# Kernel tuning notes

Measured on AMD Instinct MI355X. Metric: run time of the kernel, lower is better.

Reference implementation:

```python
import jax, jax.numpy as jnp
import numpy as np

D_MODEL = 2048
N_HEADS = 16
D_HEAD = D_MODEL // N_HEADS
BATCH = 4
SEQ = 2048


def setup_inputs() -> dict:
    key = jax.random.key(0)
    ks = jax.random.split(key, 10)
    s = 1.0 / np.sqrt(D_MODEL)
    inp = {
        "x": jax.random.normal(ks[0], (BATCH, SEQ, D_MODEL), dtype=jnp.float32),
        "attn_mask": jnp.ones((1, 1, SEQ, SEQ), dtype=jnp.int32),
        "Wq": jax.random.uniform(ks[1], (D_MODEL, D_MODEL), jnp.float32, -s, s),
        "bq": jax.random.uniform(ks[2], (D_MODEL,), jnp.float32, -s, s),
        "Wk": jax.random.uniform(ks[3], (D_MODEL, D_MODEL), jnp.float32, -s, s),
        "bk": jax.random.uniform(ks[4], (D_MODEL,), jnp.float32, -s, s),
        "Wv": jax.random.uniform(ks[5], (D_MODEL, D_MODEL), jnp.float32, -s, s),
        "bv": jax.random.uniform(ks[6], (D_MODEL,), jnp.float32, -s, s),
        "Wo": jax.random.uniform(ks[7], (D_MODEL, D_MODEL), jnp.float32, -s, s),
        "bo": jax.random.uniform(ks[8], (D_MODEL,), jnp.float32, -s, s),
    }
    return inp


def reference(x, attn_mask, Wq, bq, Wk, bk, Wv, bv, Wo, bo):
    B, S, D = x.shape
    # projections (torch Linear: x @ W.T + b); split heads -> (B, H, S, Dh)
    def split(t):
        return t.reshape(B, S, N_HEADS, D_HEAD).transpose(0, 2, 1, 3)
    q = split(x @ Wq.T + bq)
    k = split(x @ Wk.T + bk)
    v = split(x @ Wv.T + bv)
    scale = 1.0 / np.sqrt(D_HEAD).astype(np.float32)
    scores = jnp.einsum('bhqd,bhkd->bhqk', q, k) * scale  # (B,H,S,S)
    scores = jnp.where(attn_mask == 0, jnp.float32(-jnp.inf), scores)
    attn = jax.nn.softmax(scores, axis=-1)
    out = jnp.einsum('bhqk,bhkd->bhqd', attn, v)  # (B,H,S,Dh)
    out = out.transpose(0, 2, 1, 3).reshape(B, S, D)
    return out @ Wo.T + bo
```

## Files before the change

### kernel.cpp

```cpp
#include <hip/hip_runtime.h>
#include <stdint.h>
#include <stddef.h>

typedef __attribute__((ext_vector_type(8))) short short8;
typedef __attribute__((ext_vector_type(4))) float f32x4;

#define SEQ    2048
#define DMODEL 2048
#define NHEAD  16
#define DHEAD  128
#define BATCH  4
#define KVT    32
#define NKVT   (SEQ / KVT)

__device__ __forceinline__ unsigned short f2b(float f) {
  unsigned int u;
  __builtin_memcpy(&u, &f, sizeof(u));
  u = u + 0x7FFFu + ((u >> 16) & 1u);
  return (unsigned short)(u >> 16);
}

__device__ __forceinline__ void gload16(const void* g, void* l) {
  __builtin_amdgcn_global_load_lds(
      (const __attribute__((address_space(1))) unsigned int*)g,
      (__attribute__((address_space(3))) unsigned int*)l, 16, 0, 0);
}


__global__ __launch_bounds__(256) void cvt_x_kernel(
    const float* __restrict__ src, unsigned short* __restrict__ dst, int n8)
{
  const int idx = blockIdx.x * 256 + threadIdx.x;
  if (idx >= n8) return;
  const f32x4 a = *(const f32x4*)(src + (size_t)idx * 8);
  const f32x4 b = *(const f32x4*)(src + (size_t)idx * 8 + 4);
  short8 o;
  o[0] = (short)f2b(a[0]); o[1] = (short)f2b(a[1]);
  o[2] = (short)f2b(a[2]); o[3] = (short)f2b(a[3]);
  o[4] = (short)f2b(b[0]); o[5] = (short)f2b(b[1]);
  o[6] = (short)f2b(b[2]); o[7] = (short)f2b(b[3]);
  const int i = idx >> 8;
  const int k = (idx & 255) * 8;
  const size_t e = ((size_t)(i >> 4) * 64 + (k >> 5)) * 512
                 + (((k >> 3) & 3) * 16 + (i & 15)) * 8;
  *(short8*)(dst + e) = o;
}

__global__ __launch_bounds__(256) void cvt_w_kernel(
    const float* __restrict__ s0, const float* __restrict__ s1,
    const float* __restrict__ s2, const float* __restrict__ s3,
    unsigned short* __restrict__ dst, int n8)
{
  const int y = blockIdx.y;
  const float* src = (y == 0) ? s0 : (y == 1) ? s1 : (y == 2) ? s2 : s3;
  unsigned short* d = dst + (size_t)y * DMODEL * DMODEL;
  const int idx = blockIdx.x * 256 + threadIdx.x;
  if (idx >= n8) return;
  const f32x4 a = *(const f32x4*)(src + (size_t)idx * 8);
  const f32x4 b = *(const f32x4*)(src + (size_t)idx * 8 + 4);
  short8 o;
  o[0] = (short)f2b(a[0]); o[1] = (short)f2b(a[1]);
  o[2] = (short)f2b(a[2]); o[3] = (short)f2b(a[3]);
  o[4] = (short)f2b(b[0]); o[5] = (short)f2b(b[1]);
  o[6] = (short)f2b(b[2]); o[7] = (short)f2b(b[3]);
  const int i = idx >> 8;
  const int k = (idx & 255) * 8;
  const size_t e = ((size_t)(i >> 4) * 64 + (k >> 5)) * 512
                 + (((k >> 3) & 3) * 16 + (i & 15)) * 8;
  *(short8*)(d + e) = o;
}

__global__ __launch_bounds__(512, 2) void gemm_bt_kernel(
    const unsigned short* __restrict__ A,
    const unsigned short* __restrict__ W0, const unsigned short* __restrict__ W1,
    const unsigned short* __restrict__ W2,
    const float* __restrict__ b0, const float* __restrict__ b1,
    const float* __restrict__ b2,
    unsigned short* __restrict__ o0, unsigned short* __restrict__ o1,
    unsigned short* __restrict__ o2,
    float* __restrict__ of,
    int mode_base)
{
  const int z = blockIdx.z;
  const unsigned short* W    = (z == 0) ? W0 : (z == 1) ? W1 : W2;
  const float* bias          = (z == 0) ? b0 : (z == 1) ? b1 : b2;
  unsigned short* out        = (z == 0) ? o0 : (z == 1) ? o1 : o2;
  const int mode = mode_base + z;

  const int mt = blockIdx.x * 4 + (blockIdx.y & 3);
  const int nt = blockIdx.y >> 2;
  const int m0 = mt * 256;
  const int n0 = nt * 256;

  __shared__ __align__(16) unsigned short LA[4][8192];
  __shared__ __align__(16) unsigned short LB[4][8192];

  const int tid = threadIdx.x;
  const int wid = tid >> 6;
  const int ln  = tid & 63;
  const int l15 = ln & 15;
  const int lg  = ln >> 4;
  const int wr  = wid >> 2;
  const int wc  = wid & 3;

  const unsigned short* sA = A + ((size_t)((m0 >> 4) + wid) * 64) * 512 + ln * 8;
  const unsigned short* sB = W + ((size_t)((n0 >> 4) + wid) * 64) * 512 + ln * 8;
  const size_t FROW8 = (size_t)8 * 64 * 512;

  auto stage = [&](int kt) {
    unsigned short* dA = &LA[kt & 3][wid * 512 + ln * 8];
    unsigned short* dB = &LB[kt & 3][wid * 512 + ln * 8];
    gload16(sA + (size_t)kt * 512,         dA);
    gload16(sA + FROW8 + (size_t)kt * 512, dA + 8 * 512);
    gload16(sB + (size_t)kt * 512,         dB);
    gload16(sB + FROW8 + (size_t)kt * 512, dB + 8 * 512);
  };

  f32x4 acc[8][4];
#pragma unroll
  for (int m = 0; m < 8; ++m)
#pragma unroll
    for (int n = 0; n < 4; ++n) acc[m][n] = (f32x4){0.f, 0.f, 0.f, 0.f};

  stage(0); stage(1); stage(2);
  asm volatile("s_waitcnt vmcnt(8)" ::: "memory");
  __builtin_amdgcn_s_barrier();
  asm volatile("" ::: "memory");

  for (int j = 0; j < 64; ++j) {
    const int buf = j & 3;

    short8 bfr[4], a[8];
#pragma unroll
    for (int ni = 0; ni < 4; ++ni)
      bfr[ni] = *(const short8*)(&LB[buf][(wc * 4 + ni) * 512 + ln * 8]);
#pragma unroll
    for (int mi = 0; mi < 8; ++mi)
      a[mi] = *(const short8*)(&LA[buf][(wr * 8 + mi) * 512 + ln * 8]);

    if (j + 3 < 64) stage(j + 3);

    __builtin_amdgcn_s_setprio(1);
#pragma unroll
    for (int mi = 0; mi < 8; ++mi)
#pragma unroll
      for (int ni = 0; ni < 4; ++ni)
        acc[mi][ni] = __builtin_amdgcn_mfma_f32_16x16x32_bf16(a[mi], bfr[ni], acc[mi][ni], 0, 0, 0);
    __builtin_amdgcn_s_setprio(0);

    if (j <= 60)      asm volatile("s_waitcnt vmcnt(8)" ::: "memory");
    else if (j == 61) asm volatile("s_waitcnt vmcnt(4)" ::: "memory");
    else if (j == 62) asm volatile("s_waitcnt vmcnt(0)" ::: "memory");
    asm volatile("" ::: "memory");
    __builtin_amdgcn_s_barrier();
    asm volatile("" ::: "memory");
  }

#pragma unroll
  for (int n = 0; n < 4; ++n) {
    const int jj = n0 + wc * 64 + n * 16 + l15;
    const float bb = bias[jj];
#pragma unroll
    for (int m = 0; m < 8; ++m) {
#pragma unroll
      for (int r = 0; r < 4; ++r) {
        const int i = m0 + wr * 128 + m * 16 + lg * 4 + r;
        float v = acc[m][n][r] + bb;
        if (mode == 0) v *= 0.0883883476483184f;
        if (mode == 3) {
          of[(size_t)i * DMODEL + jj] = v;
        } else {
          const int b = i >> 11, s = i & 2047, hh = jj >> 7, dh = jj & 127;
          const size_t bhOff = (size_t)(b * 16 + hh) * (SEQ * DHEAD);
          size_t addr;
          if (mode == 0)
            addr = bhOff + (size_t)s * DHEAD + dh;
          else if (mode == 1)
            addr = bhOff + (size_t)(s >> 4) * 2048 + (dh >> 5) * 512
                 + ((dh >> 3) & 3) * 128 + (s & 15) * 8 + (dh & 7);
          else
            addr = bhOff + (size_t)(s >> 5) * 4096 + (dh >> 4) * 512
                 + ((s >> 3) & 3) * 128 + (dh & 15) * 8 + (s & 7);
          out[addr] = f2b(v);
        }
      }
    }
  }
}

__global__ __launch_bounds__(256, 4) void attn_kernel(
    const unsigned short* __restrict__ Q,
    const unsigned short* __restrict__ Kf,
    const unsigned short* __restrict__ Vf,
    unsigned short* __restrict__ AO)
{
  const int idx = blockIdx.x;
  const int xcd = idx & 7;
  const int sq  = idx >> 3;
  const int bh  = xcd * 8 + (sq >> 5);
  const int qt  = sq & 31;

  const int wave = threadIdx.x >> 6;
  const int lane = threadIdx.x & 63;
  const int l15  = lane & 15;
  const int lg   = lane >> 4;
  const int q0   = qt * 64 + wave * 16;

  const unsigned short* Qb = Q  + (size_t)bh * SEQ * DHEAD;
  const unsigned short* Kb = Kf + (size_t)bh * SEQ * DHEAD;
  const unsigned short* Vb = Vf + (size_t)bh * SEQ * DHEAD;

  __shared__ __align__(16) unsigned short Ks[2][4096];
  __shared__ __align__(16) unsigned short Vs[2][4096];
  __shared__ __align__(16) unsigned short P[4][16][40];

  short8 qf[4];
#pragma unroll
  for (int k = 0; k < 4; ++k)
    qf[k] = *(const short8*)(Qb + (size_t)(q0 + l15) * DHEAD + k * 32 + lg * 8);

  short8 onesf;
#pragma unroll
  for (int e = 0; e < 8; ++e) onesf[e] = (short)0x3F80;

  f32x4 oacc[9];
#pragma unroll
  for (int n = 0; n < 9; ++n) oacc[n] = (f32x4){0.f, 0.f, 0.f, 0.f};
  float mrun[4];
#pragma unroll
  for (int r = 0; r < 4; ++r) mrun[r] = -1e30f;

  const int t = threadIdx.x;
  auto STAGE = [&](int buf, int kvt) {
    const unsigned short* ksrc = Kb + (size_t)kvt * 4096;
    const unsigned short* vsrc = Vb + (size_t)kvt * 4096;
    gload16(ksrc + t * 8,        &Ks[buf][t * 8]);
    gload16(ksrc + 2048 + t * 8, &Ks[buf][2048 + t * 8]);
    gload16(vsrc + t * 8,        &Vs[buf][t * 8]);
    gload16(vsrc + 2048 + t * 8, &Vs[buf][2048 + t * 8]);
  };

  STAGE(0, 0);

  for (int kvt = 0; kvt < NKVT; ++kvt) {
    const int cur = kvt & 1;
    if (kvt + 1 < NKVT) {
      STAGE(cur ^ 1, kvt + 1);
      asm volatile("s_waitcnt vmcnt(4)" ::: "memory");
    } else {
      asm volatile("s_waitcnt vmcnt(0)" ::: "memory");
    }
    __builtin_amdgcn_s_barrier();
    __builtin_amdgcn_sched_barrier(0);

    f32x4 sacc[2];
#pragma unroll
    for (int n = 0; n < 2; ++n) sacc[n] = (f32x4){0.f, 0.f, 0.f, 0.f};
    __builtin_amdgcn_s_setprio(1);
#pragma unroll
    for (int n = 0; n < 2; ++n) {
#pragma unroll
      for (int k = 0; k < 4; ++k) {
        short8 kfr = *(const short8*)(&Ks[cur][n * 2048 + k * 512 + lane * 8]);
        sacc[n] = __builtin_amdgcn_mfma_f32_16x16x32_bf16(qf[k], kfr, sacc[n], 0, 0, 0);
      }
    }
    __builtin_amdgcn_s_setprio(0);

    float d = -1e30f;
#pragma unroll
    for (int r = 0; r < 4; ++r)
      d = fmaxf(d, fmaxf(sacc[0][r], sacc[1][r]) - mrun[r]);
    if (__any(d > 8.f)) {
#pragma unroll
      for (int r = 0; r < 4; ++r) {
        float m = fmaxf(sacc[0][r], sacc[1][r]);
        m = fmaxf(m, __shfl_xor(m, 1));
        m = fmaxf(m, __shfl_xor(m, 2));
        m = fmaxf(m, __shfl_xor(m, 4));
        m = fmaxf(m, __shfl_xor(m, 8));
        if (m > mrun[r]) {
          const float alpha = __expf(mrun[r] - m);
#pragma unroll
          for (int n = 0; n < 9; ++n) oacc[n][r] *= alpha;
          mrun[r] = m;
        }
      }
    }

#pragma unroll
    for (int n = 0; n < 2; ++n)
#pragma unroll
      for (int r = 0; r < 4; ++r)
        P[wave][lg * 4 + r][n * 16 + l15] =
            (unsigned short)f2b(__expf(sacc[n][r] - mrun[r]));
    asm volatile("s_waitcnt lgkmcnt(0)" ::: "memory");
    __builtin_amdgcn_sched_barrier(0);

    short8 pf = *(const short8*)(&P[wave][l15][lg * 8]);
    __builtin_amdgcn_s_setprio(1);
#pragma unroll
    for (int n = 0; n < 8; ++n) {
      short8 vfr = *(const short8*)(&Vs[cur][n * 512 + lane * 8]);
      oacc[n] = __builtin_amdgcn_mfma_f32_16x16x32_bf16(pf, vfr, oacc[n], 0, 0, 0);
    }
    oacc[8] = __builtin_amdgcn_mfma_f32_16x16x32_bf16(pf, onesf, oacc[8], 0, 0, 0);
    __builtin_amdgcn_s_setprio(0);

    asm volatile("s_waitcnt lgkmcnt(0)" ::: "memory");
    __builtin_amdgcn_s_barrier();
    __builtin_amdgcn_sched_barrier(0);
  }

  const int b = bh >> 4, h = bh & 15;
  float inv[4];
#pragma unroll
  for (int r = 0; r < 4; ++r) inv[r] = 1.f / oacc[8][r];
#pragma unroll
  for (int n = 0; n < 8; ++n) {
    const int kk  = h * 4 + (n >> 1);
    const int sub = (n * 2 + (l15 >> 3)) & 3;
#pragma unroll
    for (int r = 0; r < 4; ++r) {
      const int i = b * SEQ + q0 + lg * 4 + r;
      const size_t e = ((size_t)(i >> 4) * 64 + kk) * 512
                     + sub * 128 + (i & 15) * 8 + (l15 & 7);
      AO[e] = f2b(oacc[n][r] * inv[r]);
    }
  }
}

extern "C" void kernel_launch(void* const* d_in, const int* in_sizes, int n_in,
                              void* d_out, int out_size, void* d_ws, size_t ws_size,
                              hipStream_t stream)
{
  const float* xf  = (const float*)d_in[0];
  const float* Wqf = (const float*)d_in[2];
  const float* bq  = (const float*)d_in[3];
  const float* Wkf = (const float*)d_in[4];
  const float* bk  = (const float*)d_in[5];
  const float* Wvf = (const float*)d_in[6];
  const float* bv  = (const float*)d_in[7];
  const float* Wof = (const float*)d_in[8];
  const float* bo  = (const float*)d_in[9];
  float* out = (float*)d_out;

  const size_t QE = (size_t)64 * SEQ * DHEAD;
  const size_t WE = (size_t)DMODEL * DMODEL;

  unsigned short* Qw = (unsigned short*)d_out;
  unsigned short* Kw = Qw + QE;

  unsigned short* Vtw = (unsigned short*)d_ws;
  unsigned short* AOw = Vtw + QE;
  unsigned short* xb  = AOw + QE;
  unsigned short* Wb  = xb + QE;
  unsigned short* Wqb = Wb;
  unsigned short* Wkb = Wb + WE;
  unsigned short* Wvb = Wb + 2 * WE;
  unsigned short* Wob = Wb + 3 * WE;

  cvt_x_kernel<<<dim3((int)(QE / 8 / 256)), 256, 0, stream>>>(xf, xb, (int)(QE / 8));
  cvt_w_kernel<<<dim3((int)(WE / 8 / 256), 4), 256, 0, stream>>>(
      Wqf, Wkf, Wvf, Wof, Wb, (int)(WE / 8));

  gemm_bt_kernel<<<dim3(8, 32, 3), 512, 0, stream>>>(
      xb, Wqb, Wkb, Wvb, bq, bk, bv, Qw, Kw, Vtw, nullptr, 0);

  attn_kernel<<<dim3(2048), 256, 0, stream>>>(Qw, Kw, Vtw, AOw);

  gemm_bt_kernel<<<dim3(8, 32, 1), 512, 0, stream>>>(
      AOw, Wob, Wob, Wob, bo, bo, bo, nullptr, nullptr, nullptr, out, 3);
}
```

Before: 537.1 us.

## Restructure projection GEMM mainloop into half-tile ping-pong phases with split A/B staging

Reworks the projection GEMM main loop from one phase per K-tile with 3-deep prefetch into four sub-phases per pair of K-tiles. Each sub-phase loads half the A fragments, issues either the A or the B global-to-LDS copy, and runs a 4x4 MFMA block between extra barriers. The aim is to interleave LDS reads, async global loads and MFMA work more finely and to hold fewer fragment registers, in the style of ping-pong schedules. The cost is extra barriers per K-tile and a prefetch depth cut from 3 tiles to 2.

```diff
diff --git a/kernel.cpp b/kernel.cpp
--- a/kernel.cpp
+++ b/kernel.cpp
@@ -107,14 +107,16 @@
   const unsigned short* sB = W + ((size_t)((n0 >> 4) + wid) * 64) * 512 + ln * 8;
   const size_t FROW8 = (size_t)8 * 64 * 512;
 
-  auto stage = [&](int kt) {
-    unsigned short* dA = &LA[kt & 3][wid * 512 + ln * 8];
-    unsigned short* dB = &LB[kt & 3][wid * 512 + ln * 8];
-    gload16(sA + (size_t)kt * 512,         dA);
-    gload16(sA + FROW8 + (size_t)kt * 512, dA + 8 * 512);
-    gload16(sB + (size_t)kt * 512,         dB);
-    gload16(sB + FROW8 + (size_t)kt * 512, dB + 8 * 512);
+  auto stageA = [&](int h) {
+    unsigned short* dA = &LA[h & 3][wid * 512 + ln * 8];
+    gload16(sA + (size_t)h * 512,         dA);
+    gload16(sA + FROW8 + (size_t)h * 512, dA + 8 * 512);
   };
+  auto stageB = [&](int h) {
+    unsigned short* dB = &LB[h & 3][wid * 512 + ln * 8];
+    gload16(sB + (size_t)h * 512,         dB);
+    gload16(sB + FROW8 + (size_t)h * 512, dB + 8 * 512);
+  };
 
   f32x4 acc[8][4];
 #pragma unroll
@@ -122,38 +124,79 @@
 #pragma unroll
     for (int n = 0; n < 4; ++n) acc[m][n] = (f32x4){0.f, 0.f, 0.f, 0.f};
 
-  stage(0); stage(1); stage(2);
-  asm volatile("s_waitcnt vmcnt(8)" ::: "memory");
+  stageA(0); stageB(0); stageA(1); stageB(1);
+  asm volatile("s_waitcnt vmcnt(4)" ::: "memory");
   __builtin_amdgcn_s_barrier();
-  asm volatile("" ::: "memory");
-
-  for (int j = 0; j < 64; ++j) {
-    const int buf = j & 3;
-
-    short8 bfr[4], a[8];
+
+  for (int j = 0; j < 32; ++j) {
+    const int h0 = j * 2, h1 = h0 + 1;
+    const int s0 = h0 & 3, s1 = h1 & 3;
+    short8 a[4], b[4];
+
 #pragma unroll
     for (int ni = 0; ni < 4; ++ni)
-      bfr[ni] = *(const short8*)(&LB[buf][(wc * 4 + ni) * 512 + ln * 8]);
-#pragma unroll
-    for (int mi = 0; mi < 8; ++mi)
-      a[mi] = *(const short8*)(&LA[buf][(wr * 8 + mi) * 512 + ln * 8]);
-
-    if (j + 3 < 64) stage(j + 3);
-
-    __builtin_amdgcn_s_setprio(1);
-#pragma unroll
-    for (int mi = 0; mi < 8; ++mi)
+      b[ni] = *(const short8*)(&LB[s0][(wc * 4 + ni) * 512 + ln * 8]);
+#pragma unroll
+    for (int mi = 0; mi < 4; ++mi)
+      a[mi] = *(const short8*)(&LA[s0][(wr * 8 + mi) * 512 + ln * 8]);
+    if (h0 + 2 < 64) stageA(h0 + 2);
+    __builtin_amdgcn_s_barrier();
+    __builtin_amdgcn_s_setprio(1);
+#pragma unroll
+    for (int mi = 0; mi < 4; ++mi)
 #pragma unroll
       for (int ni = 0; ni < 4; ++ni)
-        acc[mi][ni] = __builtin_amdgcn_mfma_f32_16x16x32_bf16(a[mi], bfr[ni], acc[mi][ni], 0, 0, 0);
-    __builtin_amdgcn_s_setprio(0);
-
-    if (j <= 60)      asm volatile("s_waitcnt vmcnt(8)" ::: "memory");
-    else if (j == 61) asm volatile("s_waitcnt vmcnt(4)" ::: "memory");
-    else if (j == 62) asm volatile("s_waitcnt vmcnt(0)" ::: "memory");
-    asm volatile("" ::: "memory");
-    __builtin_amdgcn_s_barrier();
-    asm volatile("" ::: "memory");
+        acc[mi][ni] = __builtin_amdgcn_mfma_f32_16x16x32_bf16(a[mi], b[ni], acc[mi][ni], 0, 0, 0);
+    __builtin_amdgcn_s_setprio(0);
+    __builtin_amdgcn_s_barrier();
+
+#pragma unroll
+    for (int mi = 0; mi < 4; ++mi)
+      a[mi] = *(const short8*)(&LA[s0][(wr * 8 + 4 + mi) * 512 + ln * 8]);
+    if (h0 + 2 < 64) stageB(h0 + 2);
+    __builtin_amdgcn_s_barrier();
+    __builtin_amdgcn_s_setprio(1);
+#pragma unroll
+    for (int mi = 0; mi < 4; ++mi)
+#pragma unroll
+      for (int ni = 0; ni < 4; ++ni)
+        acc[4 + mi][ni] = __builtin_amdgcn_mfma_f32_16x16x32_bf16(a[mi], b[ni], acc[4 + mi][ni], 0, 0, 0);
+    __builtin_amdgcn_s_setprio(0);
+    if (j < 31) asm volatile("s_waitcnt vmcnt(4)" ::: "memory");
+    else        asm volatile("s_waitcnt vmcnt(0)" ::: "memory");
+    __builtin_amdgcn_s_barrier();
+
+#pragma unroll
+    for (int ni = 0; ni < 4; ++ni)
+      b[ni] = *(const short8*)(&LB[s1][(wc * 4 + ni) * 512 + ln * 8]);
+#pragma unroll
+    for (int mi = 0; mi < 4; ++mi)
+      a[mi] = *(const short8*)(&LA[s1][(wr * 8 + mi) * 512 + ln * 8]);
+    if (h1 + 2 < 64) stageA(h1 + 2);
+    __builtin_amdgcn_s_barrier();
+    __builtin_amdgcn_s_setprio(1);
+#pragma unroll
+    for (int mi = 0; mi < 4; ++mi)
+#pragma unroll
+      for (int ni = 0; ni < 4; ++ni)
+        acc[mi][ni] = __builtin_amdgcn_mfma_f32_16x16x32_bf16(a[mi], b[ni], acc[mi][ni], 0, 0, 0);
+    __builtin_amdgcn_s_setprio(0);
+    __builtin_amdgcn_s_barrier();
+
+#pragma unroll
+    for (int mi = 0; mi < 4; ++mi)
+      a[mi] = *(const short8*)(&LA[s1][(wr * 8 + 4 + mi) * 512 + ln * 8]);
+    if (h1 + 2 < 64) stageB(h1 + 2);
+    __builtin_amdgcn_s_barrier();
+    __builtin_amdgcn_s_setprio(1);
+#pragma unroll
+    for (int mi = 0; mi < 4; ++mi)
+#pragma unroll
+      for (int ni = 0; ni < 4; ++ni)
+        acc[4 + mi][ni] = __builtin_amdgcn_mfma_f32_16x16x32_bf16(a[mi], b[ni], acc[4 + mi][ni], 0, 0, 0);
+    __builtin_amdgcn_s_setprio(0);
+    if (j < 31) asm volatile("s_waitcnt vmcnt(4)" ::: "memory");
+    __builtin_amdgcn_s_barrier();
   }
 
 #pragma unroll
```

Measured after the change: 561.0 us. +4.4%, slower.
